# Optimization experiments

Measured on AMD Instinct MI355X. Metric: run time of the kernel, lower is better.

## Reference

```python
import jax, jax.numpy as jnp
import numpy as np

N_NODES = 50000
N_EDGES = 800000
NODE_IN = 256
EDGE_OUT = 64
GLOBAL_IN = 128
NODE_OUT = 256
HIDDEN = 512
N_GRAPHS = 64


def setup_inputs() -> dict:
    key = jax.random.key(0)
    ks = jax.random.split(key, 8)
    x = jax.random.normal(ks[0], (N_NODES, NODE_IN), dtype=jnp.float32)
    edge_index = jax.random.randint(ks[1], (2, N_EDGES), 0, N_NODES, dtype=jnp.int64)
    edge_attr = jax.random.normal(ks[2], (N_EDGES, EDGE_OUT), dtype=jnp.float32)
    u = jax.random.normal(ks[3], (N_GRAPHS, GLOBAL_IN), dtype=jnp.float32)
    batch = jnp.sort(jax.random.randint(ks[4], (N_NODES,), 0, N_GRAPHS, dtype=jnp.int64))
    in_dim = NODE_IN + EDGE_OUT + GLOBAL_IN
    # MLP params (torch nn.Linear default init: U(-1/sqrt(fan_in), 1/sqrt(fan_in)))
    b1s = 1.0 / np.sqrt(in_dim)
    b2s = 1.0 / np.sqrt(HIDDEN)
    W1 = jax.random.uniform(ks[5], (in_dim, HIDDEN), dtype=jnp.float32, minval=-b1s, maxval=b1s)
    b1 = jnp.zeros((HIDDEN,), dtype=jnp.float32)
    W2 = jax.random.uniform(ks[6], (HIDDEN, NODE_OUT), dtype=jnp.float32, minval=-b2s, maxval=b2s)
    b2 = jnp.zeros((NODE_OUT,), dtype=jnp.float32)
    return {"x": x, "edge_index": edge_index, "edge_attr": edge_attr, "u": u,
            "batch": batch, "W1": W1, "b1": b1, "W2": W2, "b2": b2}


def reference(x, edge_index, edge_attr, u, batch, W1, b1, W2, b2):
    n = x.shape[0]
    src = edge_index[0]
    # scatter_mean(edge_attr, src, dim=0, dim_size=n)
    sums = jax.ops.segment_sum(edge_attr, src, num_segments=n)          # [N, E_out]
    counts = jax.ops.segment_sum(jnp.ones((edge_attr.shape[0],), edge_attr.dtype),
                                 src, num_segments=n)                   # [N]
    edge_attr_agg = sums / jnp.maximum(counts, 1.0)[:, None]
    u_expanded = u[batch]                                               # [N, G_in]
    combined = jnp.concatenate([x, edge_attr_agg, u_expanded], axis=1)  # [N, 448]
    h = jax.nn.relu(combined @ W1 + b1)                                 # [N, H]
    return h @ W2 + b2                                                  # [N, N_out]
```

## Files before the change

### kernel.cpp

```cpp
#include <hip/hip_runtime.h>
#include <hip/hip_bf16.h>
#include <stdint.h>

#define NN 50000
#define NE 800000
#define NODE_IN 256
#define EDGE_OUT 64
#define GLOBAL_IN 128
#define NODE_OUT 256
#define HIDDEN 512
#define K1 320
#define N_GRAPHS 64
#define MAXDEG 64

typedef __attribute__((ext_vector_type(8))) short bf16x8;
typedef __attribute__((ext_vector_type(4))) float f32x4;
typedef __attribute__((ext_vector_type(4))) unsigned short us4;

__device__ __forceinline__ unsigned short f2bf(float x) {
    union { float f; unsigned int u; } c; c.f = x;
    unsigned int u = c.u;
    unsigned int r = (u + 0x7FFFu + ((u >> 16) & 1u)) >> 16;
    return (unsigned short)r;
}

#define GLD_LDS(gp, lp) __builtin_amdgcn_global_load_lds( \
    (const __attribute__((address_space(1))) unsigned int*)(gp), \
    (__attribute__((address_space(3))) unsigned int*)(lp), 16, 0, 0)

#define PREP_W1 (HIDDEN * K1)
#define PREP_W2 (PREP_W1 + NODE_OUT * HIDDEN)
#define PREP_G  (PREP_W2 + N_GRAPHS * HIDDEN)
#define PREP_Z  (PREP_G + NN)
__global__ __launch_bounds__(256)
void prep(const float* __restrict__ W1, const float* __restrict__ W2,
          const float* __restrict__ u, const float* __restrict__ b1,
          unsigned short* __restrict__ W1T, unsigned short* __restrict__ W2T,
          float* __restrict__ G, int* __restrict__ cnt)
{
    int idx = blockIdx.x * 256 + threadIdx.x;
    if (idx < PREP_W1) {
        int n = idx / K1, k = idx - n * K1;
        W1T[idx] = f2bf(W1[(size_t)k * HIDDEN + n]);
    } else if (idx < PREP_W2) {
        int j = idx - PREP_W1;
        int n = j / HIDDEN, k = j - n * HIDDEN;
        W2T[j] = f2bf(W2[(size_t)k * NODE_OUT + n]);
    } else if (idx < PREP_G) {
        int j = idx - PREP_W2;
        int g = j >> 9, col = j & 511;
        const float* up = u + (size_t)g * GLOBAL_IN;
        float acc = b1[col];
        #pragma unroll 4
        for (int k = 0; k < GLOBAL_IN; ++k)
            acc += up[k] * W1[(size_t)(K1 + k) * HIDDEN + col];
        G[j] = acc;
    } else if (idx < PREP_Z) {
        cnt[idx - PREP_G] = 0;
    }
}

__global__ __launch_bounds__(256)
void fill_perm(const int* __restrict__ src, int* __restrict__ cnt,
               int* __restrict__ perm)
{
    int e = blockIdx.x * 256 + threadIdx.x;
    if (e < NE) {
        int s = src[e];
        int pos = atomicAdd(&cnt[s], 1);
        if (pos < MAXDEG) perm[(size_t)s * MAXDEG + pos] = e;
    }
}

__global__ __launch_bounds__(256)
void seg_comb(const float* __restrict__ edge_attr,
              const int* __restrict__ perm,
              const int* __restrict__ cnt,
              const float* __restrict__ x,
              unsigned short* __restrict__ comb)
{
    int node = blockIdx.x * 4 + (threadIdx.x >> 6);
    if (node >= NN) return;
    int lane = threadIdx.x & 63;
    unsigned short* crow = comb + (size_t)node * K1;

    {
        const float4 v = *(const float4*)(x + (size_t)node * NODE_IN + lane * 4);
        us4 o = { f2bf(v.x), f2bf(v.y), f2bf(v.z), f2bf(v.w) };
        *(us4*)(crow + lane * 4) = o;
    }
    int c = cnt[node];
    int cc = c < MAXDEG ? c : MAXDEG;
    int g = lane >> 4;
    int f = (lane & 15) * 4;
    const int* pbase = perm + (size_t)node * MAXDEG;
    float4 acc = make_float4(0.f, 0.f, 0.f, 0.f);
    for (int i = g; i < cc; i += 4) {
        int e = pbase[i];
        const float4 v = *(const float4*)(edge_attr + (size_t)e * EDGE_OUT + f);
        acc.x += v.x; acc.y += v.y; acc.z += v.z; acc.w += v.w;
    }
    #pragma unroll
    for (int off = 16; off < 64; off <<= 1) {
        acc.x += __shfl_xor(acc.x, off, 64);
        acc.y += __shfl_xor(acc.y, off, 64);
        acc.z += __shfl_xor(acc.z, off, 64);
        acc.w += __shfl_xor(acc.w, off, 64);
    }
    if (g == 0) {
        float inv = 1.0f / fmaxf((float)c, 1.0f);
        us4 o = { f2bf(acc.x * inv), f2bf(acc.y * inv),
                  f2bf(acc.z * inv), f2bf(acc.w * inv) };
        *(us4*)(crow + NODE_IN + f) = o;
    }
}

template<int EPI>
__global__ __launch_bounds__(256)
void gemm_bt_128(const unsigned short* __restrict__ A,
                 const unsigned short* __restrict__ B,
                 const float* __restrict__ bias,
                 const int* __restrict__ batch,
                 void* __restrict__ Cv,
                 int M, int N, int K)
{
    __shared__ unsigned short lA[128 * 32];
    __shared__ unsigned short lB[128 * 32];
    const int tid = threadIdx.x;
    const int w = tid >> 6, l = tid & 63;

    const int nwg  = gridDim.x * gridDim.y;
    const int orig = blockIdx.x + gridDim.x * blockIdx.y;
    const int q = nwg >> 3, r = nwg & 7;
    const int xcd = orig & 7, sidx = orig >> 3;
    const int wg = (xcd < r ? xcd * (q + 1) : r * (q + 1) + (xcd - r) * q) + sidx;
    const int m0 = (wg / gridDim.x) * 128;
    const int n0 = (wg % gridDim.x) * 128;

    const int wr = w >> 1, wc = w & 1;

    f32x4 acc[4][4] = {};

    const int cA0 = w * 64 + l;
    const int cA1 = cA0 + 256;
    const int rA0 = cA0 >> 2, kA0 = (((cA0 & 3) ^ (rA0 & 3)) * 8);
    const int rA1 = cA1 >> 2, kA1 = (((cA1 & 3) ^ (rA1 & 3)) * 8);
    int gr0 = m0 + rA0; if (gr0 >= M) gr0 = M - 1;
    int gr1 = m0 + rA1; if (gr1 >= M) gr1 = M - 1;
    const unsigned short* pA0 = A + (size_t)gr0 * K + kA0;
    const unsigned short* pA1 = A + (size_t)gr1 * K + kA1;
    const unsigned short* pB0 = B + (size_t)(n0 + rA0) * K + kA0;
    const unsigned short* pB1 = B + (size_t)(n0 + rA1) * K + kA1;

    const int lko = (l >> 4) * 8;

    for (int k0 = 0; k0 < K; k0 += 32) {
        GLD_LDS(pA0 + k0, &lA[(size_t)cA0 * 8]);
        GLD_LDS(pA1 + k0, &lA[(size_t)cA1 * 8]);
        GLD_LDS(pB0 + k0, &lB[(size_t)cA0 * 8]);
        GLD_LDS(pB1 + k0, &lB[(size_t)cA1 * 8]);
        __syncthreads();

        bf16x8 af[4], bfr[4];
        #pragma unroll
        for (int m = 0; m < 4; ++m) {
            int ar = wr * 64 + m * 16 + (l & 15);
            af[m] = *(const bf16x8*)&lA[ar * 32 + (lko ^ ((ar & 3) << 3))];
        }
        #pragma unroll
        for (int n = 0; n < 4; ++n) {
            int br = wc * 64 + n * 16 + (l & 15);
            bfr[n] = *(const bf16x8*)&lB[br * 32 + (lko ^ ((br & 3) << 3))];
        }

        #pragma unroll
        for (int m = 0; m < 4; ++m)
            #pragma unroll
            for (int n = 0; n < 4; ++n)
                acc[m][n] = __builtin_amdgcn_mfma_f32_16x16x32_bf16(af[m], bfr[n], acc[m][n], 0, 0, 0);

        __syncthreads();
    }

    const int cbase = n0 + wc * 64 + (l & 15);
    const int rbase = m0 + wr * 64 + ((l >> 4) << 2);
    if (EPI == 0) {
        unsigned short* C = (unsigned short*)Cv;
        #pragma unroll
        for (int m = 0; m < 4; ++m) {
            #pragma unroll
            for (int j = 0; j < 4; ++j) {
                int row = rbase + m * 16 + j;
                if (row < M) {
                    const float* grow = bias + (size_t)batch[row] * HIDDEN;
                    #pragma unroll
                    for (int n = 0; n < 4; ++n) {
                        int c = cbase + n * 16;
                        float v = acc[m][n][j] + grow[c];
                        v = fmaxf(v, 0.0f);
                        C[(size_t)row * N + c] = f2bf(v);
                    }
                }
            }
        }
    } else {
        float* C = (float*)Cv;
        #pragma unroll
        for (int m = 0; m < 4; ++m) {
            #pragma unroll
            for (int j = 0; j < 4; ++j) {
                int row = rbase + m * 16 + j;
                if (row < M) {
                    #pragma unroll
                    for (int n = 0; n < 4; ++n) {
                        int c = cbase + n * 16;
                        C[(size_t)row * N + c] = acc[m][n][j] + bias[c];
                    }
                }
            }
        }
    }
}

extern "C" void kernel_launch(void* const* d_in, const int* in_sizes, int n_in,
                              void* d_out, int out_size, void* d_ws, size_t ws_size,
                              hipStream_t stream)
{
    const float* x         = (const float*)d_in[0];
    const int*   edge_idx  = (const int*)d_in[1];
    const float* edge_attr = (const float*)d_in[2];
    const float* u         = (const float*)d_in[3];
    const int*   batch     = (const int*)d_in[4];
    const float* W1        = (const float*)d_in[5];
    const float* b1        = (const float*)d_in[6];
    const float* W2        = (const float*)d_in[7];
    const float* b2        = (const float*)d_in[8];
    float* out = (float*)d_out;

    char* ws = (char*)d_ws;
    int*            cnt    = (int*)(ws);
    int*            perm   = (int*)(ws + 200704);
    unsigned short* comb   = (unsigned short*)(ws + 13000704);
    unsigned short* W1T    = (unsigned short*)(ws + 45000704);
    unsigned short* W2T    = (unsigned short*)(ws + 45328384);
    float*          G      = (float*)(ws + 45590528);
    unsigned short* h      = (unsigned short*)(ws + 45721600);

    prep<<<(PREP_Z + 255) / 256, 256, 0, stream>>>(W1, W2, u, b1, W1T, W2T, G, cnt);

    fill_perm<<<(NE + 255) / 256, 256, 0, stream>>>(edge_idx, cnt, perm);

    seg_comb<<<(NN + 3) / 4, 256, 0, stream>>>(edge_attr, perm, cnt, x, comb);

    gemm_bt_128<0><<<dim3(HIDDEN / 128, (NN + 127) / 128), 256, 0, stream>>>(
        comb, W1T, G, batch, h, NN, HIDDEN, K1);
    gemm_bt_128<1><<<dim3(NODE_OUT / 128, (NN + 127) / 128), 256, 0, stream>>>(
        h, W2T, b2, nullptr, out, NN, NODE_OUT, HIDDEN);
}
```

Measured before the change: 221.3 us.

## Double GEMM K-tile to 64 with 8-way swizzle and unroll edge gather loop

The GEMM main loop now stages a 64-wide K slice per iteration instead of 32, with a new 8-granule XOR swizzle, and runs two MFMA sub-steps per barrier pair. This halves the number of __syncthreads and global-to-LDS round trips, at the cost of double the LDS footprint, which may reduce occupancy. The edge-attribute aggregation loop is also unrolled by two with separate accumulators so more gathered loads are in flight per lane.

```diff
diff --git a/kernel.cpp b/kernel.cpp
--- a/kernel.cpp
+++ b/kernel.cpp
@@ -94,12 +94,23 @@
     int g = lane >> 4;
     int f = (lane & 15) * 4;
     const int* pbase = perm + (size_t)node * MAXDEG;
-    float4 acc = make_float4(0.f, 0.f, 0.f, 0.f);
-    for (int i = g; i < cc; i += 4) {
-        int e = pbase[i];
-        const float4 v = *(const float4*)(edge_attr + (size_t)e * EDGE_OUT + f);
-        acc.x += v.x; acc.y += v.y; acc.z += v.z; acc.w += v.w;
-    }
+    float4 a0 = make_float4(0.f, 0.f, 0.f, 0.f);
+    float4 a1 = make_float4(0.f, 0.f, 0.f, 0.f);
+    int i = g;
+    for (; i + 4 < cc; i += 8) {
+        int e0 = pbase[i];
+        int e1 = pbase[i + 4];
+        const float4 v0 = *(const float4*)(edge_attr + (size_t)e0 * EDGE_OUT + f);
+        const float4 v1 = *(const float4*)(edge_attr + (size_t)e1 * EDGE_OUT + f);
+        a0.x += v0.x; a0.y += v0.y; a0.z += v0.z; a0.w += v0.w;
+        a1.x += v1.x; a1.y += v1.y; a1.z += v1.z; a1.w += v1.w;
+    }
+    if (i < cc) {
+        int e0 = pbase[i];
+        const float4 v0 = *(const float4*)(edge_attr + (size_t)e0 * EDGE_OUT + f);
+        a0.x += v0.x; a0.y += v0.y; a0.z += v0.z; a0.w += v0.w;
+    }
+    float4 acc = make_float4(a0.x + a1.x, a0.y + a1.y, a0.z + a1.z, a0.w + a1.w);
     #pragma unroll
     for (int off = 16; off < 64; off <<= 1) {
         acc.x += __shfl_xor(acc.x, off, 64);
@@ -124,8 +135,8 @@
                  void* __restrict__ Cv,
                  int M, int N, int K)
 {
-    __shared__ unsigned short lA[128 * 32];
-    __shared__ unsigned short lB[128 * 32];
+    __shared__ unsigned short lA[128 * 64];
+    __shared__ unsigned short lB[128 * 64];
     const int tid = threadIdx.x;
     const int w = tid >> 6, l = tid & 63;
 
@@ -141,44 +152,48 @@
 
     f32x4 acc[4][4] = {};
 
-    const int cA0 = w * 64 + l;
-    const int cA1 = cA0 + 256;
-    const int rA0 = cA0 >> 2, kA0 = (((cA0 & 3) ^ (rA0 & 3)) * 8);
-    const int rA1 = cA1 >> 2, kA1 = (((cA1 & 3) ^ (rA1 & 3)) * 8);
-    int gr0 = m0 + rA0; if (gr0 >= M) gr0 = M - 1;
-    int gr1 = m0 + rA1; if (gr1 >= M) gr1 = M - 1;
-    const unsigned short* pA0 = A + (size_t)gr0 * K + kA0;
-    const unsigned short* pA1 = A + (size_t)gr1 * K + kA1;
-    const unsigned short* pB0 = B + (size_t)(n0 + rA0) * K + kA0;
-    const unsigned short* pB1 = B + (size_t)(n0 + rA1) * K + kA1;
-
-    const int lko = (l >> 4) * 8;
-
-    for (int k0 = 0; k0 < K; k0 += 32) {
-        GLD_LDS(pA0 + k0, &lA[(size_t)cA0 * 8]);
-        GLD_LDS(pA1 + k0, &lA[(size_t)cA1 * 8]);
-        GLD_LDS(pB0 + k0, &lB[(size_t)cA0 * 8]);
-        GLD_LDS(pB1 + k0, &lB[(size_t)cA1 * 8]);
+    const unsigned short* pAs[4];
+    const unsigned short* pBs[4];
+    #pragma unroll
+    for (int i = 0; i < 4; ++i) {
+        int c = tid + i * 256;
+        int row = c >> 3;
+        int kg = ((c & 7) ^ (row & 7)) * 8;
+        int gr = m0 + row; if (gr >= M) gr = M - 1;
+        pAs[i] = A + (size_t)gr * K + kg;
+        pBs[i] = B + (size_t)(n0 + row) * K + kg;
+    }
+
+    for (int k0 = 0; k0 < K; k0 += 64) {
+        #pragma unroll
+        for (int i = 0; i < 4; ++i)
+            GLD_LDS(pAs[i] + k0, &lA[(size_t)(tid + i * 256) * 8]);
+        #pragma unroll
+        for (int i = 0; i < 4; ++i)
+            GLD_LDS(pBs[i] + k0, &lB[(size_t)(tid + i * 256) * 8]);
         __syncthreads();
 
-        bf16x8 af[4], bfr[4];
-        #pragma unroll
-        for (int m = 0; m < 4; ++m) {
-            int ar = wr * 64 + m * 16 + (l & 15);
-            af[m] = *(const bf16x8*)&lA[ar * 32 + (lko ^ ((ar & 3) << 3))];
+        #pragma unroll
+        for (int kk = 0; kk < 2; ++kk) {
+            bf16x8 af[4], bfr[4];
+            #pragma unroll
+            for (int m = 0; m < 4; ++m) {
+                int ar = wr * 64 + m * 16 + (l & 15);
+                int gran = (kk * 4 + (l >> 4)) ^ (ar & 7);
+                af[m] = *(const bf16x8*)&lA[ar * 64 + gran * 8];
+            }
+            #pragma unroll
+            for (int n = 0; n < 4; ++n) {
+                int br = wc * 64 + n * 16 + (l & 15);
+                int gran = (kk * 4 + (l >> 4)) ^ (br & 7);
+                bfr[n] = *(const bf16x8*)&lB[br * 64 + gran * 8];
+            }
+            #pragma unroll
+            for (int m = 0; m < 4; ++m)
+                #pragma unroll
+                for (int n = 0; n < 4; ++n)
+                    acc[m][n] = __builtin_amdgcn_mfma_f32_16x16x32_bf16(af[m], bfr[n], acc[m][n], 0, 0, 0);
         }
-        #pragma unroll
-        for (int n = 0; n < 4; ++n) {
-            int br = wc * 64 + n * 16 + (l & 15);
-            bfr[n] = *(const bf16x8*)&lB[br * 32 + (lko ^ ((br & 3) << 3))];
-        }
-
-        #pragma unroll
-        for (int m = 0; m < 4; ++m)
-            #pragma unroll
-            for (int n = 0; n < 4; ++n)
-                acc[m][n] = __builtin_amdgcn_mfma_f32_16x16x32_bf16(af[m], bfr[n], acc[m][n], 0, 0, 0);
-
         __syncthreads();
     }
 
```

Measured after the change: 213.3 us. 1.04x faster.
